# Kernel optimization log

Measured on AMD Instinct MI355X. Metric: run time of the kernel, lower is better.

## Reference

```python
import jax, jax.numpy as jnp
import numpy as np
import math

B, H, T, D = 4, 16, 577, 1024   # CLIP ViT-L/336: 576 patches + CLS
NEED = 192                      # need_token_num
GROUP = NEED // 4               # 48 PCA components


def setup_inputs():
    key = jax.random.key(0)
    k1, k2 = jax.random.split(key)
    hidden_states = jax.random.normal(k1, (B, T, D), dtype=jnp.float32)
    attn = jax.random.uniform(k2, (B, H, T, T), dtype=jnp.float32)
    attn_weights = attn / attn.sum(-1, keepdims=True)  # row-stochastic attention
    return {"hidden_states": hidden_states, "attn_weights": attn_weights}


def batch_pca(hidden, q):
    # torch.pca_lowrank(sigmoid(h).transpose(2,1)[:,:,1:], q): center columns, top-q right singular vectors
    M = jax.nn.sigmoid(hidden.astype(jnp.float32)).transpose(0, 2, 1)[:, :, 1:]  # [B, D, N]
    Mc = M - M.mean(axis=1, keepdims=True)
    _, _, Vh = jnp.linalg.svd(Mc, full_matrices=False)      # [B, min(D,N), N]
    V = jnp.abs(jnp.transpose(Vh[:, :q, :], (0, 2, 1)))     # [B, N, q]
    belong = jnp.argmax(V, axis=-1)                          # [B, N]
    return V, belong


def batch_similarity_nms(group_sim, scores, threshold):
    # group_sim [B,G,N,N], scores [B,N,G], threshold [B]
    Bn, G, N, _ = group_sim.shape
    bi = jnp.arange(Bn)[:, None]
    gi = jnp.arange(G)[None, :]

    def cond(state):
        return state[0].sum() > 0

    def body(state):
        ns, rs, counts, gs = state
        max_values = ns.max(axis=1)          # [B,G]
        max_idx = jnp.argmax(ns, axis=1)     # [B,G]
        valid = max_values > 0
        sim_row = group_sim[bi, gi, max_idx]  # [B,G,N] row of selected token
        idx_n = jnp.where(valid, max_idx, N)  # sentinel -> dropped
        rs = rs.at[bi, idx_n, gi].set(gs, mode='drop')
        ns = ns.at[bi, idx_n, gi].set(0.0, mode='drop')
        suppress = sim_row > threshold[:, None, None]          # [B,G,N]
        ns = jnp.where(jnp.transpose(suppress, (0, 2, 1)), 0.0, ns)
        return ns, rs, counts + valid.astype(jnp.int32), gs - 1.0

    init = (scores, scores, jnp.zeros((Bn, G), jnp.int32), jnp.float32(1000.0))
    _, rs, counts, _ = jax.lax.while_loop(cond, body, init)
    return counts, rs  # kept-per-group counts, return_scores


def _forward(hs, attn):
    Bn, T_, _ = hs.shape
    N = T_ - 1
    need, G = NEED, GROUP
    hsc = jax.lax.stop_gradient(hs)
    attnc = jax.lax.stop_gradient(attn)

    V, belong = batch_pca(hsc, G)
    cls_sum = attnc[:, :, 0, 1:].sum(axis=1)                  # [B,N] cls attention
    onehot = belong[:, :, None] == jnp.arange(G)[None, None, :]  # [B,N,G]
    scores = jnp.where(onehot, cls_sum[:, :, None], 0.0).astype(jnp.float32)

    x = hsc[:, 1:, :]
    normalized = x / jnp.maximum(jnp.linalg.norm(x, axis=-1, keepdims=True), 1e-12)
    similarity = jnp.einsum('bnd,bmd->bnm', normalized, normalized).astype(jnp.float32)
    triu = jnp.triu(jnp.ones((N, N), bool), k=1)
    sim_mean = (similarity * triu).sum((-1, -2)) / triu.sum()  # [B]

    m = belong[:, None, :] == jnp.arange(G)[None, :, None]     # [B,G,N]
    mask4 = m[:, :, :, None] | m[:, :, None, :]                # row-or-col in group
    group_sim = jnp.where(mask4, similarity[:, None, :, :], 0.0)  # [B,G,N,N]

    keep_counts, ret_scores = batch_similarity_nms(group_sim, scores, (need / 32.0) * sim_mean)

    group_counts = onehot.sum(axis=1).astype(jnp.int32)        # [B,G]
    lower = jnp.minimum(1, group_counts)
    upper = jnp.minimum(jnp.minimum(5 * math.ceil(need / 64), group_counts), keep_counts)

    def ub_cond(u):
        return jnp.any(u.sum(-1) < need)

    def ub_body(u):
        deficient = (u.sum(-1) < need).astype(u.dtype)
        return jnp.minimum(u + deficient[:, None], group_counts)

    upper = jax.lax.while_loop(ub_cond, ub_body, upper)

    other = jnp.maximum(need - lower.sum(-1) - 1, 0)           # [B]
    norm_counts = keep_counts.astype(jnp.float32) / keep_counts.sum(-1, keepdims=True).astype(jnp.float32)
    csum = jnp.cumsum(norm_counts, axis=-1)
    od = jnp.round(csum * other[:, None].astype(jnp.float32)).astype(jnp.int32)
    od = od - jnp.concatenate([jnp.zeros((Bn, 1), jnp.int32), od[:, :-1]], axis=-1)
    token_d0 = jnp.minimum(od + lower, upper)
    sort_idx_g = jnp.argsort(-keep_counts, axis=-1)            # groups by kept count, desc
    target = other + lower.sum(-1)                             # == need-1 per batch
    bi1 = jnp.arange(Bn)

    def f_cond(state):
        return jnp.any(state[0].sum(-1) < target)

    def f_body(state):
        d, fg = state
        deficient = d.sum(-1) < target
        gidx = jnp.take_along_axis(sort_idx_g, jnp.minimum(fg, G - 1)[:, None], axis=1)[:, 0]
        fill = jnp.minimum(upper[bi1, gidx] - d[bi1, gidx], target - d.sum(-1))
        d = d.at[bi1, gidx].add(jnp.where(deficient, fill, 0))
        return d, fg + deficient.astype(fg.dtype)

    token_d, _ = jax.lax.while_loop(f_cond, f_body, (token_d0, jnp.zeros((Bn,), jnp.int32)))

    # top token_d[b,g] indices per group by return_scores, concatenated in group order
    sort_idx = jnp.transpose(jnp.argsort(-ret_scores, axis=1), (0, 2, 1)).astype(jnp.int32)  # [B,G,N]
    take = jnp.arange(N)[None, None, :] < token_d[:, :, None]  # [B,G,N]
    flat_take = take.reshape(Bn, G * N)
    flat_idx = sort_idx.reshape(Bn, G * N)
    L = need - 1  # token_d sums exactly to target == need-1
    pos = jnp.cumsum(flat_take, axis=1) - 1
    pos = jnp.where(flat_take, pos, L)
    gathered = jnp.zeros((Bn, L), jnp.int32).at[bi1[:, None], pos].set(flat_idx, mode='drop')
    batch_indices = jnp.concatenate([jnp.zeros((Bn, 1), jnp.int32), gathered + 1], axis=1)  # [B, need]
    out = jnp.take_along_axis(hs, batch_indices[:, :, None], axis=1)  # [B, need, D]
    return out, batch_indices


def reference(hidden_states, attn_weights):
    return _forward(hidden_states, attn_weights)
```

## Files before the change

kernel.cpp:

```cpp
#include <hip/hip_runtime.h>
#include <math.h>

constexpr int B_ = 4, T_ = 577, N_ = 576, D_ = 1024, G_ = 48, H_ = 16;
constexpr int NEED_ = 192, L_ = 191;
constexpr int TRIU_CNT = N_ * (N_ - 1) / 2;
constexpr int NB_ = 8;
constexpr int NBAR_ = 640;

constexpr int TRI_BLKS = B_ * NB_;
constexpr int GM_BX = N_ / 32;
constexpr int GM_BLKS = GM_BX * GM_BX * B_;
constexpr int CLS_BLKS = (B_ * N_ + 511) / 512;
constexpr int FUSED_BLKS = TRI_BLKS + GM_BLKS + CLS_BLKS;

constexpr size_t OF_MSIG = 0;
constexpr size_t OF_SIM  = OF_MSIG + (size_t)B_*N_*D_*4;
constexpr size_t OF_A    = OF_SIM  + (size_t)B_*N_*N_*4;
constexpr size_t OF_MS   = OF_A    + (size_t)B_*N_*N_*8;
constexpr size_t OF_INVN = OF_MS   + (size_t)B_*N_*8;
constexpr size_t OF_CLS  = OF_INVN + (size_t)B_*N_*8;
constexpr size_t OF_DT   = OF_CLS  + (size_t)B_*N_*4;
constexpr size_t OF_ET   = OF_DT   + (size_t)B_*N_*8;
constexpr size_t OF_TAU  = OF_ET   + (size_t)B_*N_*8;
constexpr size_t OF_EVAL = OF_TAU  + (size_t)B_*N_*8;
constexpr size_t OF_Z    = OF_EVAL + (size_t)B_*G_*8;
constexpr size_t OF_PART = OF_Z    + (size_t)B_*G_*N_*8;
constexpr size_t OF_THR  = OF_PART + (size_t)B_*36*8;
constexpr size_t OF_BEL  = OF_THR  + 64;
constexpr size_t OF_BAR  = OF_BEL  + (size_t)B_*N_*4;
constexpr size_t OF_FLG  = OF_BAR  + (size_t)B_*NBAR_*4;
constexpr size_t OF_VB   = OF_FLG  + (size_t)B_*16*4;
constexpr size_t OF_WB   = OF_VB   + (size_t)B_*N_*8;
constexpr size_t OF_SG   = OF_WB   + (size_t)B_*2*N_*8;
constexpr size_t OF_KP   = OF_SG   + (size_t)B_*8*8;
constexpr size_t WS_NEEDED = OF_KP + (size_t)B_*2*16*8;

constexpr size_t OF_PV_ALIAS = OF_MSIG + ((size_t)8 << 20);

__device__ __forceinline__ double blockReduceD(double x, double* red) {
  int lane = threadIdx.x & 63, wv = threadIdx.x >> 6;
  int nw = (blockDim.x + 63) >> 6;
  for (int o = 32; o > 0; o >>= 1) x += __shfl_down(x, o);
  __syncthreads();
  if (lane == 0) red[wv] = x;
  __syncthreads();
  double t = red[0];
  for (int i = 1; i < nw; i++) t += red[i];
  return t;
}

__device__ __forceinline__ void blockReduce4(double& x0, double& x1, double& x2,
                                             double& x3, double* red) {
  int lane = threadIdx.x & 63, wv = threadIdx.x >> 6;
  int nw = (blockDim.x + 63) >> 6;
  for (int o = 32; o > 0; o >>= 1) {
    x0 += __shfl_down(x0, o); x1 += __shfl_down(x1, o);
    x2 += __shfl_down(x2, o); x3 += __shfl_down(x3, o);
  }
  __syncthreads();
  if (lane == 0) { red[wv*4+0]=x0; red[wv*4+1]=x1; red[wv*4+2]=x2; red[wv*4+3]=x3; }
  __syncthreads();
  double t0 = red[0], t1 = red[1], t2 = red[2], t3 = red[3];
  for (int i = 1; i < nw; i++) {
    t0 += red[i*4+0]; t1 += red[i*4+1]; t2 += red[i*4+2]; t3 += red[i*4+3];
  }
  x0 = t0; x1 = t1; x2 = t2; x3 = t3;
}

__device__ __forceinline__ double cload(const double* p) {
  return __hip_atomic_load(p, __ATOMIC_RELAXED, __HIP_MEMORY_SCOPE_AGENT);
}
__device__ __forceinline__ void cstore(double* p, double x) {
  __hip_atomic_store(p, x, __ATOMIC_RELAXED, __HIP_MEMORY_SCOPE_AGENT);
}

__device__ __forceinline__ void gbar(int* bar, int slot, int tid) {
  __syncthreads();
  if (tid == 0) {
    __hip_atomic_fetch_add(&bar[slot], 1, __ATOMIC_RELAXED, __HIP_MEMORY_SCOPE_AGENT);
    while (__hip_atomic_load(&bar[slot], __ATOMIC_ACQUIRE, __HIP_MEMORY_SCOPE_AGENT) < NB_)
      __builtin_amdgcn_s_sleep(2);
  }
  __syncthreads();
  __asm__ volatile("" ::: "memory");
}

__global__ void k_prep(const float* __restrict__ hs, float* __restrict__ msig,
                       double* __restrict__ ms, double* __restrict__ invn,
                       int* __restrict__ bars) {
  __shared__ double red[16];
  if (blockIdx.x == 0) {
    for (int i = threadIdx.x; i < B_ * NBAR_; i += blockDim.x) bars[i] = 0;
  }
  int bn = blockIdx.x; int b = bn / N_, n = bn % N_;
  const float* row = hs + ((size_t)b*T_ + (n+1)) * (size_t)D_;
  float* mrow = msig + (size_t)bn * D_;
  double ssig = 0.0, ssq = 0.0;
  for (int d = threadIdx.x; d < D_; d += blockDim.x) {
    float x = row[d];
    float sg = 1.0f / (1.0f + expf(-x));
    mrow[d] = sg;
    ssig += (double)sg;
    ssq  += (double)x * (double)x;
  }
  double tot_sig = blockReduceD(ssig, red);
  double tot_sq  = blockReduceD(ssq, red);
  if (threadIdx.x == 0) {
    ms[bn] = tot_sig;
    invn[bn] = 1.0 / fmax(sqrt(tot_sq), 1e-12);
  }
}

__global__ void k_gemm(const float* __restrict__ hs, const float* __restrict__ msig,
                       const double* __restrict__ ms, const double* __restrict__ invn,
                       double* __restrict__ Aout, float* __restrict__ sim, int mode) {
  __shared__ float As[32][17], Bs[32][17];
  int b = blockIdx.z;
  int bi0 = blockIdx.y * 32, bj0 = blockIdx.x * 32;
  const float* base = (mode == 0) ? (msig + (size_t)b*N_*D_)
                                  : (hs + ((size_t)b*T_ + 1) * (size_t)D_);
  int tid = threadIdx.x;
  int tx = tid & 15, ty = tid >> 4;
  double a00 = 0, a01 = 0, a10 = 0, a11 = 0;
  for (int k0 = 0; k0 < D_; k0 += 16) {
    int r = tid >> 4, c = tid & 15;
    As[r][c] = base[(size_t)(bi0 + r) * D_ + k0 + c];
    Bs[r][c] = base[(size_t)(bj0 + r) * D_ + k0 + c];
    int e = tid + 256; r = e >> 4; c = e & 15;
    As[r][c] = base[(size_t)(bi0 + r) * D_ + k0 + c];
    Bs[r][c] = base[(size_t)(bj0 + r) * D_ + k0 + c];
    __syncthreads();
#pragma unroll
    for (int kk = 0; kk < 16; kk++) {
      double x0 = As[2*ty][kk],   x1 = As[2*ty+1][kk];
      double y0 = Bs[2*tx][kk],   y1 = Bs[2*tx+1][kk];
      a00 += x0*y0; a01 += x0*y1; a10 += x1*y0; a11 += x1*y1;
    }
    __syncthreads();
  }
  int i0 = bi0 + 2*ty, j0 = bj0 + 2*tx;
  if (mode == 0) {
    const double* msb = ms + (size_t)b*N_;
    double* Ab = Aout + (size_t)b*N_*N_;
    const double inv1024 = 1.0 / 1024.0;
    Ab[(size_t)i0*N_ + j0]         = a00 - msb[i0]*msb[j0]*inv1024;
    Ab[(size_t)i0*N_ + j0+1]       = a01 - msb[i0]*msb[j0+1]*inv1024;
    Ab[(size_t)(i0+1)*N_ + j0]     = a10 - msb[i0+1]*msb[j0]*inv1024;
    Ab[(size_t)(i0+1)*N_ + j0+1]   = a11 - msb[i0+1]*msb[j0+1]*inv1024;
  } else {
    const double* iv = invn + (size_t)b*N_;
    float* sb = sim + (size_t)b*N_*N_;
    sb[(size_t)i0*N_ + j0]       = (float)(a00 * iv[i0]*iv[j0]);
    sb[(size_t)i0*N_ + j0+1]     = (float)(a01 * iv[i0]*iv[j0+1]);
    sb[(size_t)(i0+1)*N_ + j0]   = (float)(a10 * iv[i0+1]*iv[j0]);
    sb[(size_t)(i0+1)*N_ + j0+1] = (float)(a11 * iv[i0+1]*iv[j0+1]);
  }
}

__global__ void k_simsum(const float* __restrict__ sim, double* __restrict__ part) {
  __shared__ double red[4];
  int blk = blockIdx.x; int b = blk / 36, s = blk % 36;
  const float* sb = sim + (size_t)b*N_*N_;
  double p = 0.0;
  for (int i = s*16; i < s*16 + 16; i++) {
    const float* row = sb + (size_t)i*N_;
    for (int j = i + 1 + threadIdx.x; j < N_; j += blockDim.x) p += (double)row[j];
  }
  double t = blockReduceD(p, red);
  if (threadIdx.x == 0) part[blk] = t;
}

__global__ void k_thr(const double* __restrict__ part, float* __restrict__ thrF) {
  int b = threadIdx.x;
  if (b < B_) {
    double s = 0.0;
    for (int i = 0; i < 36; i++) s += part[b*36 + i];
    thrF[b] = 6.0f * (float)(s / (double)TRIU_CNT);
  }
}

union __align__(16) SharedU {
  struct {
    double rb[3][N_];
    double wwb[2][N_];
    double red[32];
    double nx0s;
  } tri;
  struct {
    float As[32][17];
    float Bs[32][17];
  } gm;
};

__global__ __launch_bounds__(512) void k_tridiag_mb(double* __restrict__ Aall,
    double* __restrict__ dT, double* __restrict__ eT, double* __restrict__ tauT,
    double* __restrict__ pv_all, double* __restrict__ wb_all,
    int* __restrict__ bars,
    const float* __restrict__ hs, const double* __restrict__ invn,
    float* __restrict__ sim, const float* __restrict__ attn,
    float* __restrict__ cls) {
  __shared__ SharedU sh;
  int tid = threadIdx.x;

  if (blockIdx.x >= TRI_BLKS && blockIdx.x < TRI_BLKS + GM_BLKS) {
    int gblk = blockIdx.x - TRI_BLKS;
    int bx = gblk % GM_BX, by = (gblk / GM_BX) % GM_BX, b = gblk / (GM_BX * GM_BX);
    int bi0 = by * 32, bj0 = bx * 32;
    const float* base = hs + ((size_t)b*T_ + 1) * (size_t)D_;
    float (&As)[32][17] = sh.gm.As;
    float (&Bs)[32][17] = sh.gm.Bs;
    int tx = tid & 15, ty = (tid < 256) ? (tid >> 4) : 0;
    double a00 = 0, a01 = 0, a10 = 0, a11 = 0;
    int r = tid >> 5;
    for (int k0 = 0; k0 < D_; k0 += 16) {
      int lr = tid >> 4, lc = tid & 15;
      As[lr][lc] = base[(size_t)(bi0 + lr) * D_ + k0 + lc];
      Bs[lr][lc] = base[(size_t)(bj0 + lr) * D_ + k0 + lc];
      __syncthreads();
      if (tid < 256) {
#pragma unroll
        for (int kk = 0; kk < 16; kk++) {
          double x0 = As[2*ty][kk],   x1 = As[2*ty+1][kk];
          double y0 = Bs[2*tx][kk],   y1 = Bs[2*tx+1][kk];
          a00 += x0*y0; a01 += x0*y1; a10 += x1*y0; a11 += x1*y1;
        }
      }
      __syncthreads();
    }
    if (tid < 256) {
      int i0 = bi0 + 2*ty, j0 = bj0 + 2*tx;
      const double* iv = invn + (size_t)b*N_;
      float* sb = sim + (size_t)b*N_*N_;
      sb[(size_t)i0*N_ + j0]       = (float)(a00 * iv[i0]*iv[j0]);
      sb[(size_t)i0*N_ + j0+1]     = (float)(a01 * iv[i0]*iv[j0+1]);
      sb[(size_t)(i0+1)*N_ + j0]   = (float)(a10 * iv[i0+1]*iv[j0]);
      sb[(size_t)(i0+1)*N_ + j0+1] = (float)(a11 * iv[i0+1]*iv[j0+1]);
    }
    return;
  }

  if (blockIdx.x >= TRI_BLKS + GM_BLKS) {
    int idx = (blockIdx.x - (TRI_BLKS + GM_BLKS)) * 512 + tid;
    if (idx < B_ * N_) {
      int b = idx / N_, n = idx % N_;
      float s = 0.0f;
      for (int h = 0; h < H_; h++)
        s += attn[(((size_t)b*H_ + h) * T_ + 0) * T_ + (1 + n)];
      cls[idx] = s;
    }
    return;
  }

  double (&rb)[3][N_] = sh.tri.rb;
  double (&wwb)[2][N_] = sh.tri.wwb;
  double* red = sh.tri.red;
  int blk = blockIdx.x;
  int b = blk % B_;
  int t = blk / B_;
  double* A  = Aall + (size_t)b*N_*N_;
  double* dv = dT   + (size_t)b*N_;
  double* ev = eT   + (size_t)b*N_;
  double* tv = tauT + (size_t)b*N_;
  double* pvB = pv_all + (size_t)b*2*N_;
  double* wbB = wb_all + (size_t)b*2*N_;
  int* bar = bars + b*NBAR_;
  int lane = tid & 63, wv = tid >> 6;

  double sig;
  {
    double ps = 0.0;
    if (tid == 0) sh.tri.nx0s = A[1];
    for (int j = tid; j < N_; j += 512) {
      rb[0][j] = 0.0;
      wwb[1][j] = 0.0;
      double a0 = A[j];
      rb[1][j] = a0;
      rb[2][j] = A[(size_t)N_ + j];
      if (j >= 1) ps += a0 * a0;
    }
    sig = blockReduceD(ps, red);
  }

  for (int k = 0; k < N_ - 2; k++) {
    int rot = k % 3;
    double* vp = rb[rot];
    double* vc = rb[(rot + 1) % 3];
    double* r2 = rb[(rot + 2) % 3];
    double* wp = wwb[(k & 1) ^ 1];
    double* wc = wwb[k & 1];
    double* wbk = wbB + (size_t)(k & 1) * N_;
    double* pvk = pvB + (size_t)(k & 1) * N_;

    double sigma = sig;
    double x0 = sh.tri.nx0s;
    double alpha, tauk;
    if (sigma == 0.0) { alpha = 0.0; tauk = 0.0; }
    else {
      alpha = (x0 >= 0.0) ? -sqrt(sigma) : sqrt(sigma);
      tauk = 1.0 / (sigma - alpha * x0);
    }
    if (tid == 0) {
      vc[k + 1] = x0 - alpha;
      if (t == 0) { dv[k] = vc[k]; ev[k] = alpha; tv[k] = tauk; }
    }
    __syncthreads();

    int rr = (k + 1) % NB_;
    int rofs = t - rr; if (rofs < 0) rofs += NB_;
    for (int r = (k + 1) + rofs + wv * NB_; r < N_; r += 8 * NB_) {
      double* Ar = A + (size_t)r * N_;
      double vrp = vp[r], wrp = wp[r];
      double pd = 0.0;
      int jbeg = k + 1;
      if (jbeg & 1) {
        if (lane == 0) {
          double nv = Ar[jbeg] - vrp * wp[jbeg] - wrp * vp[jbeg];
          Ar[jbeg] = nv;
          pd += nv * vc[jbeg];
        }
        jbeg++;
      }
      if (r == k + 2) {
        for (int j = jbeg + 2 * lane; j < N_; j += 128) {
          double2 av  = *(const double2*)(Ar + j);
          double2 wpv = *(const double2*)(wp + j);
          double2 vpv = *(const double2*)(vp + j);
          double2 vcv = *(const double2*)(vc + j);
          double nv0 = av.x - vrp * wpv.x - wrp * vpv.x;
          double nv1 = av.y - vrp * wpv.y - wrp * vpv.y;
          double2 st; st.x = nv0; st.y = nv1;
          *(double2*)(Ar + j) = st;
          pd += nv0 * vcv.x + nv1 * vcv.y;
          if (j > k + 1) cstore(&pvk[j], nv0);
          cstore(&pvk[j + 1], nv1);
        }
      } else {
        for (int j = jbeg + 2 * lane; j < N_; j += 128) {
          double2 av  = *(const double2*)(Ar + j);
          double2 wpv = *(const double2*)(wp + j);
          double2 vpv = *(const double2*)(vp + j);
          double2 vcv = *(const double2*)(vc + j);
          double nv0 = av.x - vrp * wpv.x - wrp * vpv.x;
          double nv1 = av.y - vrp * wpv.y - wrp * vpv.y;
          double2 st; st.x = nv0; st.y = nv1;
          *(double2*)(Ar + j) = st;
          pd += nv0 * vcv.x + nv1 * vcv.y;
        }
      }
      for (int o = 32; o > 0; o >>= 1) pd += __shfl_down(pd, o);
      if (lane == 0) cstore(&wbk[r], tauk * pd);
    }
    gbar(bar, k, tid);

    int i0 = k + 1 + tid;
    bool s0 = (i0 < N_), s1 = (i0 + 512 < N_);
    double w0 = s0 ? cload(&wbk[i0]) : 0.0;
    double w1 = s1 ? cload(&wbk[i0 + 512]) : 0.0;
    double p0 = (s0 && tid > 0) ? cload(&pvk[i0]) : 0.0;
    double p1 = s1 ? cload(&pvk[i0 + 512]) : 0.0;
    double wr1 = cload(&wbk[k + 1]);
    double wr2 = cload(&wbk[k + 2]);
    if ((k % NB_) == t)
      for (int j = k + 1 + tid; j < N_; j += 512) A[(size_t)k * N_ + j] = vc[j];
    double vc0 = s0 ? vc[i0] : 0.0;
    double vc1 = s1 ? vc[i0 + 512] : 0.0;
    double vk1 = vc[k + 1], vk2 = vc[k + 2];
    double r20 = s0 ? r2[i0] : 0.0;
    double r21 = s1 ? r2[i0 + 512] : 0.0;
    double a0v = r20 - vk1 * w0 - wr1 * vc0;
    double a1v = r21 - vk1 * w1 - wr1 * vc1;
    double kd = w0 * vc0 + w1 * vc1;
    double sa2 = 0.0, sav = 0.0, sv2 = 0.0;
    if (s0 && tid > 0) { sa2 += a0v*a0v; sav += a0v*vc0; sv2 += vc0*vc0; }
    if (s1)            { sa2 += a1v*a1v; sav += a1v*vc1; sv2 += vc1*vc1; }
    blockReduce4(kd, sa2, sav, sv2, red);
    double K = 0.5 * tauk * kd;
    double c = 2.0 * K * vk1;
    sig = sa2 + 2.0 * c * sav + c * c * sv2;
    double wk2 = wr2 - K * vk2;
    if (s0) {
      double wcj = w0 - K * vc0;
      wc[i0] = wcj;
      double nr1v = a0v + c * vc0;
      r2[i0] = nr1v;
      if (tid == 1) sh.tri.nx0s = nr1v;
      if (tid > 0) vp[i0] = p0 - vk2 * wcj - wk2 * vc0;
    }
    if (s1) {
      double wcj = w1 - K * vc1;
      wc[i0 + 512] = wcj;
      r2[i0 + 512] = a1v + c * vc1;
      vp[i0 + 512] = p1 - vk2 * wcj - wk2 * vc1;
    }
    __syncthreads();
  }

  if (t == 0 && tid == 0) {
    double* r1f = rb[((N_ - 3) + 2) % 3];
    double* r2f = rb[(N_ - 3) % 3];
    dv[N_-2] = r1f[N_-2];
    ev[N_-2] = r1f[N_-1];
    dv[N_-1] = r2f[N_-1];
    ev[N_-1] = 0.0; tv[N_-2] = 0.0; tv[N_-1] = 0.0;
  }
}

__global__ __launch_bounds__(64) void k_eigvals_ms(const double* __restrict__ dT,
    const double* __restrict__ eT, double* __restrict__ eval) {
  __shared__ double sd[N_], se2[N_];
  int blk = blockIdx.x; int b = blk / G_, j = blk % G_;
  int lane = threadIdx.x;
  for (int i = lane; i < N_; i += 64) {
    sd[i] = dT[(size_t)b*N_ + i];
    se2[i] = eT[(size_t)b*N_ + i];
  }
  __syncthreads();
  double lo = 1e300, hi = -1e300;
  for (int i = lane; i < N_; i += 64) {
    double r = ((i > 0) ? fabs(se2[i-1]) : 0.0) + ((i < N_-1) ? fabs(se2[i]) : 0.0);
    lo = fmin(lo, sd[i] - r); hi = fmax(hi, sd[i] + r);
  }
  for (int o = 32; o > 0; o >>= 1) {
    lo = fmin(lo, __shfl_xor(lo, o));
    hi = fmax(hi, __shfl_xor(hi, o));
  }
  double span = hi - lo + 1e-30;
  lo -= span * 1e-6; hi += span * 1e-6;
  __syncthreads();
  for (int i = lane; i < N_; i += 64) { double e = se2[i]; se2[i] = e * e; }
  __syncthreads();
  int target = N_ - 1 - j;
  for (int round = 0; round < 9; round++) {
    double width = hi - lo;
    double mid = lo + width * ((double)(lane + 1) / 65.0);
    double pm1 = 1.0;
    double pcur = sd[0] - mid;
    int cnt = (pcur <= 0.0) ? 1 : 0;
    if (pcur == 0.0) pcur = -1e-300;
    for (int i = 1; i < N_; i++) {
      double pnew = (sd[i] - mid) * pcur - se2[i-1] * pm1;
      bool chg = ((pnew < 0.0) != (pcur < 0.0)) || (pnew == 0.0);
      cnt += chg ? 1 : 0;
      if (pnew == 0.0) pnew = (pcur < 0.0) ? 1e-300 : -1e-300;
      pm1 = pcur; pcur = pnew;
      if ((i & 3) == 3) {
        double ap = fmax(fabs(pcur), fabs(pm1));
        double s = (ap > 1e160) ? 1e-160 : ((ap < 1e-160) ? 1e160 : 1.0);
        if (s != 1.0) {
          pcur *= s; pm1 *= s;
          if (pcur == 0.0) pcur = (pm1 < 0.0) ? 1e-300 : -1e-300;
          if (pm1 == 0.0)  pm1  = (pcur < 0.0) ? 1e-300 : -1e-300;
        }
      }
    }
    unsigned long long mask = __ballot(cnt > target);
    double nlo, nhi;
    if (mask == 0ULL) { nlo = lo + width * (64.0 / 65.0); nhi = hi; }
    else {
      int m = __ffsll(mask) - 1;
      nhi = lo + width * ((double)(m + 1) / 65.0);
      nlo = (m == 0) ? lo : lo + width * ((double)m / 65.0);
    }
    lo = nlo; hi = nhi;
  }
  if (lane == 0) eval[(size_t)b*G_ + j] = 0.5 * (lo + hi);
}

__global__ void k_eigvecs(const double* __restrict__ dT, const double* __restrict__ eT,
    const double* __restrict__ eval,
    double* __restrict__ Ud, double* __restrict__ U1, double* __restrict__ U2,
    double* __restrict__ Um, int* __restrict__ Ufl, double* __restrict__ Yv,
    double* __restrict__ Z) {
  __shared__ double sd[N_], se[N_];
  __shared__ double red0;
  __shared__ int cstart[G_];
  __shared__ double sh_ev[G_];
  int b = blockIdx.x;
  for (int i = threadIdx.x; i < N_; i += blockDim.x) {
    sd[i] = dT[(size_t)b*N_ + i]; se[i] = eT[(size_t)b*N_ + i];
  }
  if (threadIdx.x < G_) sh_ev[threadIdx.x] = eval[(size_t)b*G_ + threadIdx.x];
  __syncthreads();
  int j = threadIdx.x;
  size_t sbase = (size_t)b * N_ * G_;
  double* ud = Ud + sbase; double* u1 = U1 + sbase; double* u2 = U2 + sbase;
  double* um = Um + sbase; int* ufl = Ufl + sbase; double* yv = Yv + sbase;
  if (j < G_) {
    double lam = sh_ev[j];
    double GU = 1e-30 * (1.0 + fabs(lam));
    double ak = sd[0] - lam;
    double bk = se[0];
    for (int k = 0; k < N_ - 1; k++) {
      double sub = se[k];
      double diag1 = sd[k+1] - lam;
      double sup1 = (k < N_ - 2) ? se[k+1] : 0.0;
      double udv, u1v, u2v, umv; int flv;
      if (fabs(ak) >= fabs(sub)) {
        double piv = ak;
        if (fabs(piv) < GU) piv = (piv >= 0.0) ? GU : -GU;
        double rp = 1.0 / piv;
        double ml = sub * rp;
        udv = rp; u1v = bk; u2v = 0.0; umv = ml; flv = 0;
        ak = diag1 - ml * bk; bk = sup1;
      } else {
        double rs = 1.0 / sub;
        double ml = ak * rs;
        udv = rs; u1v = diag1; u2v = sup1; umv = ml; flv = 1;
        ak = bk - ml * diag1; bk = -ml * sup1;
      }
      ud[(size_t)k*G_+j] = udv; u1[(size_t)k*G_+j] = u1v; u2[(size_t)k*G_+j] = u2v;
      um[(size_t)k*G_+j] = umv; ufl[(size_t)k*G_+j] = flv;
    }
    { double piv = ak; if (fabs(piv) < GU) piv = (piv >= 0.0) ? GU : -GU;
      ud[(size_t)(N_-1)*G_+j] = 1.0 / piv; u1[(size_t)(N_-1)*G_+j] = 0.0; u2[(size_t)(N_-1)*G_+j] = 0.0; }
    for (int i = 0; i < N_; i++) {
      unsigned s = (unsigned)(i * 2654435761u) ^ (unsigned)((j + 1) * 40503u) ^ (unsigned)(b * 2246822519u);
      s = s * 1664525u + 1013904223u;
      s ^= s >> 16; s = s * 2246822519u;
      double rv = ((double)(s >> 8) * (1.0 / 16777216.0)) * 2.0 - 1.0;
      if (fabs(rv) < 1e-3) rv = 0.5;
      yv[(size_t)i*G_+j] = rv;
    }
    for (int it = 0; it < 3; it++) {
      if (it) {
        double mx = 0.0;
        for (int i = 0; i < N_; i++) mx = fmax(mx, fabs(yv[(size_t)i*G_+j]));
        double sc = 1.0 / fmax(mx, 1e-300);
        for (int i = 0; i < N_; i++) yv[(size_t)i*G_+j] *= sc;
      }
      double ykc = yv[0*G_ + j];
      for (int k = 0; k < N_ - 1; k++) {
        double ynx = yv[(size_t)(k+1)*G_+j];
        double yk = ykc, yk1 = ynx;
        if (ufl[(size_t)k*G_+j]) { yk = ynx; yk1 = ykc; }
        yk1 -= um[(size_t)k*G_+j] * yk;
        yv[(size_t)k*G_+j] = yk;
        ykc = yk1;
      }
      double y1, y2 = 0.0;
      { double tt = ykc * ud[(size_t)(N_-1)*G_+j];
        yv[(size_t)(N_-1)*G_+j] = tt; y1 = tt; }
      for (int k = N_ - 2; k >= 0; k--) {
        double tt = yv[(size_t)k*G_+j] - u1[(size_t)k*G_+j]*y1 - u2[(size_t)k*G_+j]*y2;
        tt *= ud[(size_t)k*G_+j];
        yv[(size_t)k*G_+j] = tt;
        y2 = y1; y1 = tt;
      }
    }
    double s2 = 0.0;
    for (int i = 0; i < N_; i++) { double tt = yv[(size_t)i*G_+j]; s2 += tt * tt; }
    double inv = 1.0 / sqrt(fmax(s2, 1e-300));
    double* Zj = Z + ((size_t)b*G_ + j) * N_;
    for (int i = 0; i < N_; i++) Zj[i] = yv[(size_t)i*G_+j] * inv;
  }
  __syncthreads();
  if (threadIdx.x == 0) {
    double tol = 1e-10 * (fabs(sh_ev[0]) + 1.0);
    cstart[0] = 0;
    for (int q = 1; q < G_; q++)
      cstart[q] = ((sh_ev[q-1] - sh_ev[q]) < tol) ? cstart[q-1] : q;
  }
  __syncthreads();
  for (int q = 1; q < G_; q++) {
    if (cstart[q] == q) continue;
    double* Zq = Z + ((size_t)b*G_ + q) * N_;
    for (int p = cstart[q]; p < q; p++) {
      double* Zp = Z + ((size_t)b*G_ + p) * N_;
      double dp = 0.0;
      for (int i = threadIdx.x; i < N_; i += blockDim.x) dp += Zq[i] * Zp[i];
      for (int o = 32; o > 0; o >>= 1) dp += __shfl_down(dp, o);
      if (threadIdx.x == 0) red0 = dp;
      __syncthreads();
      double dd = red0;
      for (int i = threadIdx.x; i < N_; i += blockDim.x) Zq[i] -= dd * Zp[i];
      __syncthreads();
    }
    double s2 = 0.0;
    for (int i = threadIdx.x; i < N_; i += blockDim.x) { double tt = Zq[i]; s2 += tt * tt; }
    for (int o = 32; o > 0; o >>= 1) s2 += __shfl_down(s2, o);
    if (threadIdx.x == 0) red0 = s2;
    __syncthreads();
    double inv = 1.0 / sqrt(fmax(red0, 1e-300));
    for (int i = threadIdx.x; i < N_; i += blockDim.x) Zq[i] *= inv;
    __syncthreads();
  }
}

__global__ __launch_bounds__(64) void k_backxf_mb(const double* __restrict__ Aall,
    const double* __restrict__ tauT, double* __restrict__ Z) {
  int blk = blockIdx.x;
  int b = blk / G_, q = blk % G_;
  const double* A = Aall + (size_t)b*N_*N_;
  const double* tau = tauT + (size_t)b*N_;
  double* Zq = Z + ((size_t)b*G_ + q) * N_;
  int lane = threadIdx.x;
  double z[9];
#pragma unroll
  for (int m = 0; m < 9; m++) z[m] = Zq[lane + 64*m];
  for (int k = N_ - 3; k >= 0; k--) {
    double t = tau[k];
    if (t == 0.0) continue;
    const double* vk = A + (size_t)k*N_;
    double vv[9]; double p = 0.0;
#pragma unroll
    for (int m = 0; m < 9; m++) {
      int i = lane + 64*m;
      double vi = (i > k) ? vk[i] : 0.0;
      vv[m] = vi; p += vi * z[m];
    }
    for (int o = 32; o > 0; o >>= 1) p += __shfl_down(p, o);
    p = __shfl(p, 0);
    double s = t * p;
#pragma unroll
    for (int m = 0; m < 9; m++) z[m] -= s * vv[m];
  }
#pragma unroll
  for (int m = 0; m < 9; m++) Zq[lane + 64*m] = z[m];
}

__global__ void k_belong(const double* __restrict__ Z, int* __restrict__ belong) {
  int idx = blockIdx.x * blockDim.x + threadIdx.x;
  if (idx >= B_ * N_) return;
  int b = idx / N_, n = idx % N_;
  const double* Zb = Z + (size_t)b*G_*N_;
  double best = -1.0; int bi = 0;
  for (int q = 0; q < G_; q++) {
    double av = fabs(Zb[(size_t)q*N_ + n]);
    if (av > best) { best = av; bi = q; }
  }
  belong[idx] = bi;
}

__global__ __launch_bounds__(256) void k_nms(const float* __restrict__ sim,
    const float* __restrict__ cls, const int* __restrict__ belong,
    const float* __restrict__ thrF, float* __restrict__ outF) {
  __shared__ float nsv[N_], rsv[N_];
  __shared__ int bl_s[N_];
  __shared__ int lists[N_];
  __shared__ int off[G_ + 1];
  __shared__ int kc[G_], gc[G_], lowv[G_], upv[G_], tokd[G_], sortg[G_], pre[G_ + 1];
  __shared__ int gathered[L_];
  __shared__ int anyv;
  __shared__ float shthr;
  int b = blockIdx.x, tid = threadIdx.x;
  const float* simb = sim + (size_t)b*N_*N_;
  if (tid == 0) shthr = thrF[b];
  if (tid < G_) gc[tid] = 0;
  __syncthreads();
  for (int i = tid; i < N_; i += 256) {
    int g = belong[b*N_ + i];
    bl_s[i] = g;
    float sc = cls[b*N_ + i];
    nsv[i] = sc; rsv[i] = sc;
    atomicAdd(&gc[g], 1);
  }
  __syncthreads();
  if (tid == 0) {
    off[0] = 0;
    for (int g = 0; g < G_; g++) off[g+1] = off[g] + gc[g];
    for (int g = 0; g < G_; g++) pre[g] = off[g];
    for (int n = 0; n < N_; n++) lists[pre[bl_s[n]]++] = n;
  }
  __syncthreads();
  float thr = shthr;
  float gs = 1000.0f;
  int myc = 0;
  for (int iter = 0; iter < N_ + 8; iter++) {
    if (tid == 0) anyv = 0;
    __syncthreads();
    int m = -1;
    if (tid < G_) {
      float mx = 0.0f;
      for (int a = off[tid]; a < off[tid+1]; a++) {
        int n2 = lists[a];
        float vv = nsv[n2];
        if (vv > mx) { mx = vv; m = n2; }
      }
      if (m >= 0) anyv = 1;
    }
    __syncthreads();
    if (m >= 0) {
      rsv[m] = gs;
      nsv[m] = 0.0f;
      const float* srow = simb + (size_t)m*N_;
      for (int a = off[tid]; a < off[tid+1]; a++) {
        int n2 = lists[a];
        if (nsv[n2] > 0.0f && srow[n2] > thr) nsv[n2] = 0.0f;
      }
      myc++;
    }
    gs -= 1.0f;
    __syncthreads();
    if (!anyv) break;
  }
  if (tid < G_) kc[tid] = myc;
  __syncthreads();
  if (tid == 0) {
    int sumkc = 0; for (int g = 0; g < G_; g++) sumkc += kc[g];
    int sumlow = 0;
    for (int g = 0; g < G_; g++) {
      lowv[g] = (gc[g] < 1) ? gc[g] : 1;
      int u = 15; if (gc[g] < u) u = gc[g]; if (kc[g] < u) u = kc[g];
      upv[g] = u; sumlow += lowv[g];
    }
    int su = 0; for (int g = 0; g < G_; g++) su += upv[g];
    while (su < NEED_) {
      su = 0;
      for (int g = 0; g < G_; g++) { int u = upv[g] + 1; if (u > gc[g]) u = gc[g]; upv[g] = u; su += u; }
    }
    int other = NEED_ - sumlow - 1; if (other < 0) other = 0;
    float s = (float)sumkc;
    float c = 0.0f; int prevR = 0;
    float otherf = (float)other;
    for (int g = 0; g < G_; g++) {
      float nc = (float)kc[g] / s;
      c += nc;
      int R = (int)rintf(c * otherf);
      int od = R - prevR; prevR = R;
      int t0 = od + lowv[g]; if (t0 > upv[g]) t0 = upv[g];
      tokd[g] = t0;
    }
    for (int g = 0; g < G_; g++) sortg[g] = g;
    for (int a = 1; a < G_; a++) {
      int vIdx = sortg[a]; int key = kc[vIdx]; int p2 = a - 1;
      while (p2 >= 0 && kc[sortg[p2]] < key) { sortg[p2+1] = sortg[p2]; p2--; }
      sortg[p2+1] = vIdx;
    }
    int target = other + sumlow;
    int sumd = 0; for (int g = 0; g < G_; g++) sumd += tokd[g];
    int fg = 0;
    while (sumd < target) {
      int gi = sortg[(fg < G_-1) ? fg : (G_-1)];
      int fill = upv[gi] - tokd[gi];
      int rem = target - sumd;
      if (rem < fill) fill = rem;
      tokd[gi] += fill; sumd += fill;
      fg++;
      if (fg > 100000) break;
    }
    pre[0] = 0; for (int g = 0; g < G_; g++) pre[g+1] = pre[g] + tokd[g];
  }
  __syncthreads();
  for (int i = tid; i < L_; i += 256) gathered[i] = 0;
  __syncthreads();
  if (tid < G_) {
    int g = tid;
    int td = tokd[g], base = pre[g];
    for (int t = 0; t < td; t++) {
      float bv = -3e38f; int bn2 = 0;
      for (int a = off[g]; a < off[g+1]; a++) {
        int n2 = lists[a];
        float vv = rsv[n2];
        if (vv > bv) { bv = vv; bn2 = n2; }
      }
      rsv[bn2] = -3e38f;
      int pos = base + t;
      if (pos < L_) gathered[pos] = bn2;
    }
  }
  __syncthreads();
  if (tid < NEED_) {
    float val = (tid == 0) ? 0.0f : (float)(gathered[tid - 1] + 1);
    outF[(size_t)B_*NEED_*D_ + (size_t)b*NEED_ + tid] = val;
  }
}

__global__ void k_gather(const float* __restrict__ hs, float* __restrict__ outF) {
  int blk = blockIdx.x;
  int b = blk / NEED_, i = blk % NEED_;
  int idx = (int)outF[(size_t)B_*NEED_*D_ + (size_t)b*NEED_ + i];
  const float4* src = (const float4*)(hs + ((size_t)b*T_ + idx) * (size_t)D_);
  float4* dst = (float4*)(outF + ((size_t)b*NEED_ + i) * (size_t)D_);
  dst[threadIdx.x] = src[threadIdx.x];
}

extern "C" void kernel_launch(void* const* d_in, const int* in_sizes, int n_in,
                              void* d_out, int out_size, void* d_ws, size_t ws_size,
                              hipStream_t stream) {
  if (ws_size < WS_NEEDED) return;
  const float* hs   = (const float*)d_in[0];
  const float* attn = (const float*)d_in[1];
  float* outF = (float*)d_out;
  char* w = (char*)d_ws;
  float*  msig = (float*)(w + OF_MSIG);
  float*  sim  = (float*)(w + OF_SIM);
  double* A    = (double*)(w + OF_A);
  double* ms   = (double*)(w + OF_MS);
  double* invn = (double*)(w + OF_INVN);
  float*  cls  = (float*)(w + OF_CLS);
  double* dT   = (double*)(w + OF_DT);
  double* eT   = (double*)(w + OF_ET);
  double* tauT = (double*)(w + OF_TAU);
  double* eval = (double*)(w + OF_EVAL);
  double* Z    = (double*)(w + OF_Z);
  double* part = (double*)(w + OF_PART);
  float*  thrF = (float*)(w + OF_THR);
  int*    belong = (int*)(w + OF_BEL);
  int*    bars = (int*)(w + OF_BAR);
  double* wb   = (double*)(w + OF_WB);
  double* pv   = (double*)(w + OF_PV_ALIAS);
  double* Ud = (double*)(w + OF_MSIG);
  double* U1 = Ud + (size_t)B_*N_*G_;
  double* U2 = U1 + (size_t)B_*N_*G_;
  double* Um = U2 + (size_t)B_*N_*G_;
  double* Yv = Um + (size_t)B_*N_*G_;
  int*    Ufl = (int*)(Yv + (size_t)B_*N_*G_);

  k_prep<<<B_*N_, 256, 0, stream>>>(hs, msig, ms, invn, bars);
  k_gemm<<<dim3(N_/32, N_/32, B_), 256, 0, stream>>>(hs, msig, ms, invn, A, sim, 0);
  k_tridiag_mb<<<FUSED_BLKS, 512, 0, stream>>>(A, dT, eT, tauT, pv, wb, bars,
                                               hs, invn, sim, attn, cls);
  k_simsum<<<B_*36, 256, 0, stream>>>(sim, part);
  k_thr<<<1, 64, 0, stream>>>(part, thrF);
  k_eigvals_ms<<<B_*G_, 64, 0, stream>>>(dT, eT, eval);
  k_eigvecs<<<B_, 64, 0, stream>>>(dT, eT, eval, Ud, U1, U2, Um, Ufl, Yv, Z);
  k_backxf_mb<<<B_*G_, 64, 0, stream>>>(A, tauT, Z);
  k_belong<<<(B_*N_ + 255)/256, 256, 0, stream>>>(Z, belong);
  k_nms<<<B_, 256, 0, stream>>>(sim, cls, belong, thrF, outF);
  k_gather<<<B_*NEED_, 256, 0, stream>>>(hs, outF);
}
```

Measured before the change: 7.225 ms.

## Fold similarity sum and threshold into fused tridiag kernel via flag sync

Removes the separate k_simsum and k_thr launches and runs them as extra blocks inside the fused tridiagonalization kernel. Those blocks spin on global atomic counters until all similarity GEMM blocks, and then all partial-sum blocks, have finished. The work overlaps with the long-running tridiagonal reduction and saves two launches. Separately, both GEMM inner loops now read shared memory as float4 vectors, with rows padded to 18 floats. The spin-waits assume all producer blocks get scheduled alongside the waiting ones, which is a deadlock risk if residency is limited.

```diff
diff --git a/kernel.cpp b/kernel.cpp
--- a/kernel.cpp
+++ b/kernel.cpp
@@ -11,7 +11,8 @@
 constexpr int GM_BX = N_ / 32;
 constexpr int GM_BLKS = GM_BX * GM_BX * B_;
 constexpr int CLS_BLKS = (B_ * N_ + 511) / 512;
-constexpr int FUSED_BLKS = TRI_BLKS + GM_BLKS + CLS_BLKS;
+constexpr int SIMSUM_BLKS = B_ * 36;
+constexpr int FUSED_BLKS = TRI_BLKS + GM_BLKS + CLS_BLKS + SIMSUM_BLKS + 1;
 
 constexpr size_t OF_MSIG = 0;
 constexpr size_t OF_SIM  = OF_MSIG + (size_t)B_*N_*D_*4;
@@ -73,6 +74,12 @@
 __device__ __forceinline__ void cstore(double* p, double x) {
   __hip_atomic_store(p, x, __ATOMIC_RELAXED, __HIP_MEMORY_SCOPE_AGENT);
 }
+__device__ __forceinline__ float cloadf(const float* p) {
+  return __hip_atomic_load(p, __ATOMIC_RELAXED, __HIP_MEMORY_SCOPE_AGENT);
+}
+__device__ __forceinline__ void cstoref(float* p, float x) {
+  __hip_atomic_store(p, x, __ATOMIC_RELAXED, __HIP_MEMORY_SCOPE_AGENT);
+}
 
 __device__ __forceinline__ void gbar(int* bar, int slot, int tid) {
   __syncthreads();
@@ -87,10 +94,11 @@
 
 __global__ void k_prep(const float* __restrict__ hs, float* __restrict__ msig,
                        double* __restrict__ ms, double* __restrict__ invn,
-                       int* __restrict__ bars) {
+                       int* __restrict__ bars, int* __restrict__ flags) {
   __shared__ double red[16];
   if (blockIdx.x == 0) {
     for (int i = threadIdx.x; i < B_ * NBAR_; i += blockDim.x) bars[i] = 0;
+    for (int i = threadIdx.x; i < B_ * 16; i += blockDim.x) flags[i] = 0;
   }
   int bn = blockIdx.x; int b = bn / N_, n = bn % N_;
   const float* row = hs + ((size_t)b*T_ + (n+1)) * (size_t)D_;
@@ -114,7 +122,8 @@
 __global__ void k_gemm(const float* __restrict__ hs, const float* __restrict__ msig,
                        const double* __restrict__ ms, const double* __restrict__ invn,
                        double* __restrict__ Aout, float* __restrict__ sim, int mode) {
-  __shared__ float As[32][17], Bs[32][17];
+  __shared__ __attribute__((aligned(16))) float As[32][18];
+  __shared__ __attribute__((aligned(16))) float Bs[32][18];
   int b = blockIdx.z;
   int bi0 = blockIdx.y * 32, bj0 = blockIdx.x * 32;
   const float* base = (mode == 0) ? (msig + (size_t)b*N_*D_)
@@ -131,10 +140,19 @@
     Bs[r][c] = base[(size_t)(bj0 + r) * D_ + k0 + c];
     __syncthreads();
 #pragma unroll
-    for (int kk = 0; kk < 16; kk++) {
-      double x0 = As[2*ty][kk],   x1 = As[2*ty+1][kk];
-      double y0 = Bs[2*tx][kk],   y1 = Bs[2*tx+1][kk];
-      a00 += x0*y0; a01 += x0*y1; a10 += x1*y0; a11 += x1*y1;
+    for (int kk = 0; kk < 16; kk += 4) {
+      float4 xa = *(const float4*)&As[2*ty][kk];
+      float4 xb = *(const float4*)&As[2*ty+1][kk];
+      float4 ya = *(const float4*)&Bs[2*tx][kk];
+      float4 yb = *(const float4*)&Bs[2*tx+1][kk];
+      a00 += (double)xa.x*(double)ya.x; a01 += (double)xa.x*(double)yb.x;
+      a10 += (double)xb.x*(double)ya.x; a11 += (double)xb.x*(double)yb.x;
+      a00 += (double)xa.y*(double)ya.y; a01 += (double)xa.y*(double)yb.y;
+      a10 += (double)xb.y*(double)ya.y; a11 += (double)xb.y*(double)yb.y;
+      a00 += (double)xa.z*(double)ya.z; a01 += (double)xa.z*(double)yb.z;
+      a10 += (double)xb.z*(double)ya.z; a11 += (double)xb.z*(double)yb.z;
+      a00 += (double)xa.w*(double)ya.w; a01 += (double)xa.w*(double)yb.w;
+      a10 += (double)xb.w*(double)ya.w; a11 += (double)xb.w*(double)yb.w;
     }
     __syncthreads();
   }
@@ -157,28 +175,6 @@
   }
 }
 
-__global__ void k_simsum(const float* __restrict__ sim, double* __restrict__ part) {
-  __shared__ double red[4];
-  int blk = blockIdx.x; int b = blk / 36, s = blk % 36;
-  const float* sb = sim + (size_t)b*N_*N_;
-  double p = 0.0;
-  for (int i = s*16; i < s*16 + 16; i++) {
-    const float* row = sb + (size_t)i*N_;
-    for (int j = i + 1 + threadIdx.x; j < N_; j += blockDim.x) p += (double)row[j];
-  }
-  double t = blockReduceD(p, red);
-  if (threadIdx.x == 0) part[blk] = t;
-}
-
-__global__ void k_thr(const double* __restrict__ part, float* __restrict__ thrF) {
-  int b = threadIdx.x;
-  if (b < B_) {
-    double s = 0.0;
-    for (int i = 0; i < 36; i++) s += part[b*36 + i];
-    thrF[b] = 6.0f * (float)(s / (double)TRIU_CNT);
-  }
-}
-
 union __align__(16) SharedU {
   struct {
     double rb[3][N_];
@@ -187,8 +183,8 @@
     double nx0s;
   } tri;
   struct {
-    float As[32][17];
-    float Bs[32][17];
+    float As[32][18];
+    float Bs[32][18];
   } gm;
 };
 
@@ -198,7 +194,8 @@
     int* __restrict__ bars,
     const float* __restrict__ hs, const double* __restrict__ invn,
     float* __restrict__ sim, const float* __restrict__ attn,
-    float* __restrict__ cls) {
+    float* __restrict__ cls, int* __restrict__ flags,
+    double* __restrict__ part, float* __restrict__ thrF) {
   __shared__ SharedU sh;
   int tid = threadIdx.x;
 
@@ -207,11 +204,10 @@
     int bx = gblk % GM_BX, by = (gblk / GM_BX) % GM_BX, b = gblk / (GM_BX * GM_BX);
     int bi0 = by * 32, bj0 = bx * 32;
     const float* base = hs + ((size_t)b*T_ + 1) * (size_t)D_;
-    float (&As)[32][17] = sh.gm.As;
-    float (&Bs)[32][17] = sh.gm.Bs;
+    float (&As)[32][18] = sh.gm.As;
+    float (&Bs)[32][18] = sh.gm.Bs;
     int tx = tid & 15, ty = (tid < 256) ? (tid >> 4) : 0;
     double a00 = 0, a01 = 0, a10 = 0, a11 = 0;
-    int r = tid >> 5;
     for (int k0 = 0; k0 < D_; k0 += 16) {
       int lr = tid >> 4, lc = tid & 15;
       As[lr][lc] = base[(size_t)(bi0 + lr) * D_ + k0 + lc];
@@ -219,10 +215,19 @@
       __syncthreads();
       if (tid < 256) {
 #pragma unroll
-        for (int kk = 0; kk < 16; kk++) {
-          double x0 = As[2*ty][kk],   x1 = As[2*ty+1][kk];
-          double y0 = Bs[2*tx][kk],   y1 = Bs[2*tx+1][kk];
-          a00 += x0*y0; a01 += x0*y1; a10 += x1*y0; a11 += x1*y1;
+        for (int kk = 0; kk < 16; kk += 4) {
+          float4 xa = *(const float4*)&As[2*ty][kk];
+          float4 xb = *(const float4*)&As[2*ty+1][kk];
+          float4 ya = *(const float4*)&Bs[2*tx][kk];
+          float4 yb = *(const float4*)&Bs[2*tx+1][kk];
+          a00 += (double)xa.x*(double)ya.x; a01 += (double)xa.x*(double)yb.x;
+          a10 += (double)xb.x*(double)ya.x; a11 += (double)xb.x*(double)yb.x;
+          a00 += (double)xa.y*(double)ya.y; a01 += (double)xa.y*(double)yb.y;
+          a10 += (double)xb.y*(double)ya.y; a11 += (double)xb.y*(double)yb.y;
+          a00 += (double)xa.z*(double)ya.z; a01 += (double)xa.z*(double)yb.z;
+          a10 += (double)xb.z*(double)ya.z; a11 += (double)xb.z*(double)yb.z;
+          a00 += (double)xa.w*(double)ya.w; a01 += (double)xa.w*(double)yb.w;
+          a10 += (double)xb.w*(double)ya.w; a11 += (double)xb.w*(double)yb.w;
         }
       }
       __syncthreads();
@@ -231,15 +236,18 @@
       int i0 = bi0 + 2*ty, j0 = bj0 + 2*tx;
       const double* iv = invn + (size_t)b*N_;
       float* sb = sim + (size_t)b*N_*N_;
-      sb[(size_t)i0*N_ + j0]       = (float)(a00 * iv[i0]*iv[j0]);
-      sb[(size_t)i0*N_ + j0+1]     = (float)(a01 * iv[i0]*iv[j0+1]);
-      sb[(size_t)(i0+1)*N_ + j0]   = (float)(a10 * iv[i0+1]*iv[j0]);
-      sb[(size_t)(i0+1)*N_ + j0+1] = (float)(a11 * iv[i0+1]*iv[j0+1]);
-    }
+      cstoref(&sb[(size_t)i0*N_ + j0],       (float)(a00 * iv[i0]*iv[j0]));
+      cstoref(&sb[(size_t)i0*N_ + j0+1],     (float)(a01 * iv[i0]*iv[j0+1]));
+      cstoref(&sb[(size_t)(i0+1)*N_ + j0],   (float)(a10 * iv[i0+1]*iv[j0]));
+      cstoref(&sb[(size_t)(i0+1)*N_ + j0+1], (float)(a11 * iv[i0+1]*iv[j0+1]));
+    }
+    __syncthreads();
+    if (tid == 0)
+      __hip_atomic_fetch_add(&flags[0], 1, __ATOMIC_RELEASE, __HIP_MEMORY_SCOPE_AGENT);
     return;
   }
 
-  if (blockIdx.x >= TRI_BLKS + GM_BLKS) {
+  if (blockIdx.x >= TRI_BLKS + GM_BLKS && blockIdx.x < TRI_BLKS + GM_BLKS + CLS_BLKS) {
     int idx = (blockIdx.x - (TRI_BLKS + GM_BLKS)) * 512 + tid;
     if (idx < B_ * N_) {
       int b = idx / N_, n = idx % N_;
@@ -247,6 +255,44 @@
       for (int h = 0; h < H_; h++)
         s += attn[(((size_t)b*H_ + h) * T_ + 0) * T_ + (1 + n)];
       cls[idx] = s;
+    }
+    return;
+  }
+
+  if (blockIdx.x >= TRI_BLKS + GM_BLKS + CLS_BLKS && blockIdx.x < FUSED_BLKS - 1) {
+    if (tid == 0) {
+      while (__hip_atomic_load(&flags[0], __ATOMIC_ACQUIRE, __HIP_MEMORY_SCOPE_AGENT) < GM_BLKS)
+        __builtin_amdgcn_s_sleep(4);
+    }
+    __syncthreads();
+    int sblk = blockIdx.x - (TRI_BLKS + GM_BLKS + CLS_BLKS);
+    int b = sblk / 36, s = sblk % 36;
+    const float* sb = sim + (size_t)b*N_*N_;
+    double p = 0.0;
+    if (tid < 256) {
+      for (int i = s*16; i < s*16 + 16; i++) {
+        const float* row = sb + (size_t)i*N_;
+        for (int j = i + 1 + tid; j < N_; j += 256) p += (double)cloadf(&row[j]);
+      }
+    }
+    double tsum = blockReduceD(p, sh.tri.red);
+    if (tid == 0) {
+      cstore(&part[sblk], tsum);
+      __hip_atomic_fetch_add(&flags[1], 1, __ATOMIC_RELEASE, __HIP_MEMORY_SCOPE_AGENT);
+    }
+    return;
+  }
+
+  if (blockIdx.x == FUSED_BLKS - 1) {
+    if (tid == 0) {
+      while (__hip_atomic_load(&flags[1], __ATOMIC_ACQUIRE, __HIP_MEMORY_SCOPE_AGENT) < SIMSUM_BLKS)
+        __builtin_amdgcn_s_sleep(4);
+    }
+    __syncthreads();
+    if (tid < B_) {
+      double s = 0.0;
+      for (int i = 0; i < 36; i++) s += cload(&part[tid*36 + i]);
+      thrF[tid] = 6.0f * (float)(s / (double)TRIU_CNT);
     }
     return;
   }
@@ -797,6 +843,7 @@
   float*  thrF = (float*)(w + OF_THR);
   int*    belong = (int*)(w + OF_BEL);
   int*    bars = (int*)(w + OF_BAR);
+  int*    flags = (int*)(w + OF_FLG);
   double* wb   = (double*)(w + OF_WB);
   double* pv   = (double*)(w + OF_PV_ALIAS);
   double* Ud = (double*)(w + OF_MSIG);
@@ -806,12 +853,11 @@
   double* Yv = Um + (size_t)B_*N_*G_;
   int*    Ufl = (int*)(Yv + (size_t)B_*N_*G_);
 
-  k_prep<<<B_*N_, 256, 0, stream>>>(hs, msig, ms, invn, bars);
+  k_prep<<<B_*N_, 256, 0, stream>>>(hs, msig, ms, invn, bars, flags);
   k_gemm<<<dim3(N_/32, N_/32, B_), 256, 0, stream>>>(hs, msig, ms, invn, A, sim, 0);
   k_tridiag_mb<<<FUSED_BLKS, 512, 0, stream>>>(A, dT, eT, tauT, pv, wb, bars,
-                                               hs, invn, sim, attn, cls);
-  k_simsum<<<B_*36, 256, 0, stream>>>(sim, part);
-  k_thr<<<1, 64, 0, stream>>>(part, thrF);
+                                               hs, invn, sim, attn, cls,
+                                               flags, part, thrF);
   k_eigvals_ms<<<B_*G_, 64, 0, stream>>>(dT, eT, eval);
   k_eigvecs<<<B_, 64, 0, stream>>>(dT, eT, eval, Ud, U1, U2, Um, Ufl, Yv, Z);
   k_backxf_mb<<<B_*G_, 64, 0, stream>>>(A, tauT, Z);
```

Result: no change. 7.282 ms (+0.8%).
